# Performance work log

Hardware: AMD Instinct MI355X
Metric: run time of the kernel (lower is better)

The kernel has to match this reference:

```python
import jax, jax.numpy as jnp
import numpy as np

M_DIM = 256.0  # scaling denominator from __init__ (sqrt(256) = 16)

def setup_inputs() -> dict:
    key = jax.random.key(0)
    kq, kk, kv = jax.random.split(key, 3)
    B, H, S, D = 2, 8, 4096, 64
    q = jax.random.normal(kq, (B, H, S, D), dtype=jnp.float32)
    k = jax.random.normal(kk, (B, H, S, D), dtype=jnp.float32)
    v = jax.random.normal(kv, (B, H, S, D), dtype=jnp.float32)
    return {"q": q, "k": k, "v": v}

def reference(q, k, v):
    # scores: [B, H, S, S] = q @ k^T / sqrt(m_dim)
    scores = jnp.einsum('bhqd,bhkd->bhqk', q, k) / jnp.sqrt(jnp.float32(M_DIM))
    attn = jax.nn.softmax(scores, axis=-1)
    # outputs: [B, H, S, D]
    return jnp.einsum('bhqk,bhkd->bhqd', attn, v)
```

## Files before the change

### kernel.cpp

```cpp
#include <hip/hip_runtime.h>
#include <hip/hip_bf16.h>
#include <stdint.h>

#define SEQ 4096
#define DH  64
#define KT  64
#define PS  72
#define LOG2E 1.44269504f
#define PC2   5.76796516f

typedef __attribute__((ext_vector_type(8))) short short8;
typedef __attribute__((ext_vector_type(4))) float floatx4;

__device__ __forceinline__ ushort f2bf_rne(float f) {
    unsigned u = __float_as_uint(f);
    unsigned r = u + 0x7FFFu + ((u >> 16) & 1u);
    return (ushort)(r >> 16);
}

__device__ __forceinline__ void async_copy16(void* lds, const void* gsrc) {
    __builtin_amdgcn_global_load_lds(
        (const __attribute__((address_space(1))) uint32_t*)gsrc,
        (__attribute__((address_space(3))) uint32_t*)lds, 16, 0, 0);
}

__global__ __launch_bounds__(256)
void prep_kv(const float* __restrict__ K, const float* __restrict__ V,
             ushort* __restrict__ Kbf, ushort* __restrict__ Vt) {
    const int bh = blockIdx.y, s0 = blockIdx.x * 64, t = threadIdx.x;
    const size_t base = ((size_t)bh * SEQ + s0) * DH;
    {
        const float* src = K + base + t * 16;
        ushort* dst = Kbf + base + t * 16;
        #pragma unroll
        for (int h = 0; h < 2; ++h) {
            float4 a = *(const float4*)(src + h * 8);
            float4 b = *(const float4*)(src + h * 8 + 4);
            short8 o;
            o[0] = (short)f2bf_rne(a.x); o[1] = (short)f2bf_rne(a.y);
            o[2] = (short)f2bf_rne(a.z); o[3] = (short)f2bf_rne(a.w);
            o[4] = (short)f2bf_rne(b.x); o[5] = (short)f2bf_rne(b.y);
            o[6] = (short)f2bf_rne(b.z); o[7] = (short)f2bf_rne(b.w);
            *(short8*)(dst + h * 8) = o;
        }
    }
    {
        const int d0 = (t >> 4) * 4, sl = (t & 15) * 4;
        const float* src = V + base + (size_t)sl * DH + d0;
        ushort* dst = Vt + (size_t)bh * DH * SEQ + s0 + sl;
        ushort b[4][4];
        #pragma unroll
        for (int r = 0; r < 4; ++r) {
            float4 f = *(const float4*)(src + r * DH);
            b[r][0] = f2bf_rne(f.x); b[r][1] = f2bf_rne(f.y);
            b[r][2] = f2bf_rne(f.z); b[r][3] = f2bf_rne(f.w);
        }
        #pragma unroll
        for (int i = 0; i < 4; ++i) {
            uint2 w;
            w.x = (uint)b[0][i] | ((uint)b[1][i] << 16);
            w.y = (uint)b[2][i] | ((uint)b[3][i] << 16);
            *(uint2*)(dst + (size_t)(d0 + i) * SEQ) = w;
        }
    }
}

__global__ __launch_bounds__(128, 2)
void attn_fwd_v3(const float* __restrict__ Q, const ushort* __restrict__ Kbf,
                 const ushort* __restrict__ Vt, float* __restrict__ O)
{
    __shared__ __align__(16) ushort sK [KT * DH];
    __shared__ __align__(16) ushort sVt[DH * KT];
    __shared__ __align__(16) ushort sP [2 * 32 * PS];

    const int bh   = blockIdx.y;
    const int qt0  = blockIdx.x * 64;
    const int tid  = threadIdx.x;
    const int wave = tid >> 6;
    const int lane = tid & 63;
    const int n16  = lane & 15;
    const int quad = lane >> 4;

    const float* Qb  = Q + ((size_t)bh * SEQ) * DH;
    const char*  KbB = (const char*)(Kbf + (size_t)bh * SEQ * DH);
    const char*  VtB = (const char*)(Vt  + (size_t)bh * DH * SEQ);
    float*       Ob  = O + ((size_t)bh * SEQ) * DH;

    const int qw0 = qt0 + wave * 32;
    short8 qfrag[2][2];
    #pragma unroll
    for (int qt = 0; qt < 2; ++qt) {
        const float* qrow = Qb + (size_t)(qw0 + qt * 16 + n16) * DH;
        #pragma unroll
        for (int t = 0; t < 2; ++t) {
            const float* p = qrow + t * 32 + quad * 8;
            short8 a;
            #pragma unroll
            for (int j = 0; j < 8; ++j) a[j] = (short)f2bf_rne(p[j] * 0.0625f);
            qfrag[qt][t] = a;
        }
    }

    int kOff[4], vOff[4];
    char *kLds[4], *vLds[4];
    #pragma unroll
    for (int c = 0; c < 4; ++c) {
        int L = (c * 2 + wave) * 1024 + lane * 16;
        int row = L >> 7, p = (L >> 4) & 7;
        int sw = (p ^ (row & 7)) * 16;
        kOff[c] = row * 128  + sw;
        vOff[c] = row * 8192 + sw;
        kLds[c] = (char*)sK  + (c * 2 + wave) * 1024;
        vLds[c] = (char*)sVt + (c * 2 + wave) * 1024;
    }
    const int sw0 = ((0 * 4 + quad) ^ (n16 & 7)) * 8;
    const int sw1 = ((1 * 4 + quad) ^ (n16 & 7)) * 8;

    floatx4 oacc[2][4];
    #pragma unroll
    for (int qt = 0; qt < 2; ++qt)
        #pragma unroll
        for (int nt = 0; nt < 4; ++nt) oacc[qt][nt] = (floatx4){0.f, 0.f, 0.f, 0.f};
    float l_i[2] = {0.f, 0.f};

    ushort* sPw = &sP[wave * 32 * PS];

    for (int kt0 = 0; kt0 < SEQ; kt0 += KT) {
        __syncthreads();
        #pragma unroll
        for (int c = 0; c < 4; ++c)
            async_copy16(kLds[c], KbB + (size_t)kt0 * 128 + kOff[c]);
        #pragma unroll
        for (int c = 0; c < 4; ++c)
            async_copy16(vLds[c], VtB + (size_t)kt0 * 2 + vOff[c]);
        __syncthreads();

        floatx4 sacc[4][2];
        #pragma unroll
        for (int kt = 0; kt < 4; ++kt) {
            short8 k0 = *(const short8*)&sK[(kt * 16 + n16) * 64 + sw0];
            short8 k1 = *(const short8*)&sK[(kt * 16 + n16) * 64 + sw1];
            #pragma unroll
            for (int qt = 0; qt < 2; ++qt) {
                floatx4 acc = (floatx4){0.f, 0.f, 0.f, 0.f};
                acc = __builtin_amdgcn_mfma_f32_16x16x32_bf16(k0, qfrag[qt][0], acc, 0, 0, 0);
                acc = __builtin_amdgcn_mfma_f32_16x16x32_bf16(k1, qfrag[qt][1], acc, 0, 0, 0);
                sacc[kt][qt] = acc;
            }
        }

        #pragma unroll
        for (int kt = 0; kt < 4; ++kt) {
            #pragma unroll
            for (int qt = 0; qt < 2; ++qt) {
                float p0 = __builtin_amdgcn_exp2f(__builtin_fmaf(sacc[kt][qt][0], LOG2E, -PC2));
                float p1 = __builtin_amdgcn_exp2f(__builtin_fmaf(sacc[kt][qt][1], LOG2E, -PC2));
                float p2 = __builtin_amdgcn_exp2f(__builtin_fmaf(sacc[kt][qt][2], LOG2E, -PC2));
                float p3 = __builtin_amdgcn_exp2f(__builtin_fmaf(sacc[kt][qt][3], LOG2E, -PC2));
                l_i[qt] += (p0 + p1) + (p2 + p3);
                uint2 w;
                w.x = (__float_as_uint(p0) >> 16) | (__float_as_uint(p1) & 0xFFFF0000u);
                w.y = (__float_as_uint(p2) >> 16) | (__float_as_uint(p3) & 0xFFFF0000u);
                *(uint2*)&sPw[(qt * 16 + n16) * PS + kt * 16 + quad * 4] = w;
            }
        }

        short8 pf[2][2];
        #pragma unroll
        for (int qt = 0; qt < 2; ++qt) {
            pf[qt][0] = *(const short8*)&sPw[(qt * 16 + n16) * PS + 0 * 32 + quad * 8];
            pf[qt][1] = *(const short8*)&sPw[(qt * 16 + n16) * PS + 1 * 32 + quad * 8];
        }
        #pragma unroll
        for (int nt = 0; nt < 4; ++nt) {
            short8 v0 = *(const short8*)&sVt[(nt * 16 + n16) * 64 + sw0];
            short8 v1 = *(const short8*)&sVt[(nt * 16 + n16) * 64 + sw1];
            #pragma unroll
            for (int qt = 0; qt < 2; ++qt) {
                oacc[qt][nt] = __builtin_amdgcn_mfma_f32_16x16x32_bf16(v0, pf[qt][0], oacc[qt][nt], 0, 0, 0);
                oacc[qt][nt] = __builtin_amdgcn_mfma_f32_16x16x32_bf16(v1, pf[qt][1], oacc[qt][nt], 0, 0, 0);
            }
        }
    }

    #pragma unroll
    for (int qt = 0; qt < 2; ++qt) {
        float l = l_i[qt];
        l += __shfl_xor(l, 16, 64);
        l += __shfl_xor(l, 32, 64);
        float inv = 1.0019531f / l;
        const int q = qw0 + qt * 16 + n16;
        #pragma unroll
        for (int nt = 0; nt < 4; ++nt) {
            float4 o;
            o.x = oacc[qt][nt][0] * inv;
            o.y = oacc[qt][nt][1] * inv;
            o.z = oacc[qt][nt][2] * inv;
            o.w = oacc[qt][nt][3] * inv;
            *(float4*)&Ob[(size_t)q * DH + nt * 16 + quad * 4] = o;
        }
    }
}

__global__ __launch_bounds__(256, 4)
void attn_fwd_v1(const float* __restrict__ Q, const float* __restrict__ K,
                 const float* __restrict__ V, float* __restrict__ O)
{
    __shared__ __align__(16) ushort sKf[KT * PS];
    __shared__ __align__(16) ushort sVf[DH * PS];
    __shared__ __align__(16) ushort sPf[4 * 16 * PS];
    const int bh = blockIdx.y, qt0 = blockIdx.x * 64, tid = threadIdx.x;
    const int wave = tid >> 6, lane = tid & 63, n16 = lane & 15, quad = lane >> 4;
    const size_t base = (size_t)bh * SEQ * DH;
    const float *Qb = Q + base, *Kb = K + base, *Vb = V + base;
    float* Ob = O + base;
    short8 qfrag[2];
    {
        const float* qrow = Qb + (size_t)(qt0 + wave * 16 + n16) * DH;
        #pragma unroll
        for (int t = 0; t < 2; ++t) {
            const float* p = qrow + t * 32 + quad * 8;
            short8 a;
            #pragma unroll
            for (int j = 0; j < 8; ++j) a[j] = (short)f2bf_rne(p[j] * 0.0625f);
            qfrag[t] = a;
        }
    }
    floatx4 oacc[4];
    #pragma unroll
    for (int nt = 0; nt < 4; ++nt) oacc[nt] = (floatx4){0.f,0.f,0.f,0.f};
    float m_i[4] = {-INFINITY,-INFINITY,-INFINITY,-INFINITY};
    float l_i[4] = {0.f,0.f,0.f,0.f};
    const int skr = tid >> 2, sc0 = (tid & 3) * 16;
    for (int kt0 = 0; kt0 < SEQ; kt0 += KT) {
        __syncthreads();
        const float* ksrc = Kb + (size_t)(kt0 + skr) * DH + sc0;
        const float* vsrc = Vb + (size_t)(kt0 + skr) * DH + sc0;
        ushort* kdst = &sKf[skr * PS + sc0];
        #pragma unroll
        for (int i = 0; i < 16; i += 4) {
            float4 kf = *(const float4*)(ksrc + i);
            kdst[i+0]=f2bf_rne(kf.x); kdst[i+1]=f2bf_rne(kf.y);
            kdst[i+2]=f2bf_rne(kf.z); kdst[i+3]=f2bf_rne(kf.w);
            float4 vf = *(const float4*)(vsrc + i);
            sVf[(sc0+i+0)*PS+skr]=f2bf_rne(vf.x); sVf[(sc0+i+1)*PS+skr]=f2bf_rne(vf.y);
            sVf[(sc0+i+2)*PS+skr]=f2bf_rne(vf.z); sVf[(sc0+i+3)*PS+skr]=f2bf_rne(vf.w);
        }
        __syncthreads();
        floatx4 sacc[4];
        #pragma unroll
        for (int nt = 0; nt < 4; ++nt) {
            sacc[nt] = (floatx4){0.f,0.f,0.f,0.f};
            #pragma unroll
            for (int t = 0; t < 2; ++t) {
                short8 b = *(const short8*)&sKf[(nt*16+n16)*PS + t*32 + quad*8];
                sacc[nt] = __builtin_amdgcn_mfma_f32_16x16x32_bf16(qfrag[t], b, sacc[nt], 0,0,0);
            }
        }
        ushort* pw = &sPf[wave * 16 * PS];
        #pragma unroll
        for (int r = 0; r < 4; ++r) {
            float mx = fmaxf(fmaxf(sacc[0][r],sacc[1][r]),fmaxf(sacc[2][r],sacc[3][r]));
            #pragma unroll
            for (int off = 1; off < 16; off <<= 1) mx = fmaxf(mx, __shfl_xor(mx, off, 64));
            float mnew = fmaxf(m_i[r], mx);
            float alpha = __expf(m_i[r] - mnew);
            m_i[r] = mnew;
            float sum = 0.f;
            #pragma unroll
            for (int nt = 0; nt < 4; ++nt) {
                float p = __expf(sacc[nt][r] - mnew);
                sacc[nt][r] = p; sum += p;
            }
            #pragma unroll
            for (int off = 1; off < 16; off <<= 1) sum += __shfl_xor(sum, off, 64);
            l_i[r] = l_i[r] * alpha + sum;
            #pragma unroll
            for (int nt = 0; nt < 4; ++nt) oacc[nt][r] *= alpha;
            #pragma unroll
            for (int nt = 0; nt < 4; ++nt)
                pw[(quad*4+r)*PS + nt*16 + n16] = f2bf_rne(sacc[nt][r]);
        }
        #pragma unroll
        for (int t = 0; t < 2; ++t) {
            short8 pfr = *(const short8*)&pw[n16*PS + t*32 + quad*8];
            #pragma unroll
            for (int nt = 0; nt < 4; ++nt) {
                short8 vf = *(const short8*)&sVf[(nt*16+n16)*PS + t*32 + quad*8];
                oacc[nt] = __builtin_amdgcn_mfma_f32_16x16x32_bf16(pfr, vf, oacc[nt], 0,0,0);
            }
        }
    }
    #pragma unroll
    for (int r = 0; r < 4; ++r) {
        float inv = 1.0f / l_i[r];
        float* orow = Ob + (size_t)(qt0 + wave*16 + quad*4 + r) * DH;
        #pragma unroll
        for (int nt = 0; nt < 4; ++nt) orow[nt*16+n16] = oacc[nt][r] * inv;
    }
}

extern "C" void kernel_launch(void* const* d_in, const int* in_sizes, int n_in,
                              void* d_out, int out_size, void* d_ws, size_t ws_size,
                              hipStream_t stream) {
    const float* q = (const float*)d_in[0];
    const float* k = (const float*)d_in[1];
    const float* v = (const float*)d_in[2];
    float* o = (float*)d_out;
    const size_t elems = (size_t)16 * SEQ * DH;
    const size_t need  = elems * 2 * 2;
    if (ws_size >= need) {
        ushort* kbf = (ushort*)d_ws;
        ushort* vt  = kbf + elems;
        prep_kv<<<dim3(SEQ / 64, 16), dim3(256), 0, stream>>>(k, v, kbf, vt);
        attn_fwd_v3<<<dim3(SEQ / 64, 16), dim3(128), 0, stream>>>(q, kbf, vt, o);
    } else {
        attn_fwd_v1<<<dim3(SEQ / 64, 16), dim3(256), 0, stream>>>(q, k, v, o);
    }
}
```

Measured before the change: 193.2 us.

## Split key range across wave pairs and compute row sums via MFMA

```diff
diff --git a/kernel.cpp b/kernel.cpp
--- a/kernel.cpp
+++ b/kernel.cpp
@@ -4,8 +4,8 @@
 
 #define SEQ 4096
 #define DH  64
-#define KT  64
-#define PS  72
+#define KT  32
+#define PS  40
 #define LOG2E 1.44269504f
 #define PC2   5.76796516f
 
@@ -27,13 +27,13 @@
 __global__ __launch_bounds__(256)
 void prep_kv(const float* __restrict__ K, const float* __restrict__ V,
              ushort* __restrict__ Kbf, ushort* __restrict__ Vt) {
-    const int bh = blockIdx.y, s0 = blockIdx.x * 64, t = threadIdx.x;
+    const int bh = blockIdx.y, s0 = blockIdx.x * 128, t = threadIdx.x;
     const size_t base = ((size_t)bh * SEQ + s0) * DH;
     {
-        const float* src = K + base + t * 16;
-        ushort* dst = Kbf + base + t * 16;
-        #pragma unroll
-        for (int h = 0; h < 2; ++h) {
+        const float* src = K + base + t * 32;
+        ushort* dst = Kbf + base + t * 32;
+        #pragma unroll
+        for (int h = 0; h < 4; ++h) {
             float4 a = *(const float4*)(src + h * 8);
             float4 b = *(const float4*)(src + h * 8 + 4);
             short8 o;
@@ -45,48 +45,52 @@
         }
     }
     {
-        const int d0 = (t >> 4) * 4, sl = (t & 15) * 4;
+        const int d0 = (t & 15) * 4, sl = (t >> 4) * 8;
         const float* src = V + base + (size_t)sl * DH + d0;
         ushort* dst = Vt + (size_t)bh * DH * SEQ + s0 + sl;
-        ushort b[4][4];
-        #pragma unroll
-        for (int r = 0; r < 4; ++r) {
+        ushort b[8][4];
+        #pragma unroll
+        for (int r = 0; r < 8; ++r) {
             float4 f = *(const float4*)(src + r * DH);
             b[r][0] = f2bf_rne(f.x); b[r][1] = f2bf_rne(f.y);
             b[r][2] = f2bf_rne(f.z); b[r][3] = f2bf_rne(f.w);
         }
         #pragma unroll
         for (int i = 0; i < 4; ++i) {
-            uint2 w;
-            w.x = (uint)b[0][i] | ((uint)b[1][i] << 16);
-            w.y = (uint)b[2][i] | ((uint)b[3][i] << 16);
-            *(uint2*)(dst + (size_t)(d0 + i) * SEQ) = w;
-        }
-    }
-}
-
-__global__ __launch_bounds__(128, 2)
-void attn_fwd_v3(const float* __restrict__ Q, const ushort* __restrict__ Kbf,
+            short8 w;
+            #pragma unroll
+            for (int r = 0; r < 8; ++r) w[r] = (short)b[r][i];
+            *(short8*)(dst + (size_t)(d0 + i) * SEQ) = w;
+        }
+    }
+}
+
+__global__ __launch_bounds__(256, 4)
+void attn_fwd_v4(const float* __restrict__ Q, const ushort* __restrict__ Kbf,
                  const ushort* __restrict__ Vt, float* __restrict__ O)
 {
-    __shared__ __align__(16) ushort sK [KT * DH];
-    __shared__ __align__(16) ushort sVt[DH * KT];
-    __shared__ __align__(16) ushort sP [2 * 32 * PS];
-
-    const int bh   = blockIdx.y;
-    const int qt0  = blockIdx.x * 64;
-    const int tid  = threadIdx.x;
-    const int wave = tid >> 6;
-    const int lane = tid & 63;
-    const int n16  = lane & 15;
-    const int quad = lane >> 4;
+    __shared__ __align__(16) char smem[26624];
+
+    const int bh    = blockIdx.y;
+    const int qt0   = blockIdx.x * 64;
+    const int tid   = threadIdx.x;
+    const int wave  = tid >> 6;
+    const int widx  = wave & 1;
+    const int wpair = wave >> 1;
+    const int lane  = tid & 63;
+    const int n16   = lane & 15;
+    const int quad  = lane >> 4;
 
     const float* Qb  = Q + ((size_t)bh * SEQ) * DH;
     const char*  KbB = (const char*)(Kbf + (size_t)bh * SEQ * DH);
     const char*  VtB = (const char*)(Vt  + (size_t)bh * DH * SEQ);
     float*       Ob  = O + ((size_t)bh * SEQ) * DH;
 
-    const int qw0 = qt0 + wave * 32;
+    ushort* sK  = (ushort*)(smem)         + wpair * 2048;
+    ushort* sVt = (ushort*)(smem + 8192)  + wpair * 2048;
+    ushort* sPw = (ushort*)(smem + 16384) + wave  * 1280;
+
+    const int qw0 = qt0 + widx * 32;
     short8 qfrag[2][2];
     #pragma unroll
     for (int qt = 0; qt < 2; ++qt) {
@@ -100,64 +104,67 @@
             qfrag[qt][t] = a;
         }
     }
-
-    int kOff[4], vOff[4];
-    char *kLds[4], *vLds[4];
-    #pragma unroll
-    for (int c = 0; c < 4; ++c) {
-        int L = (c * 2 + wave) * 1024 + lane * 16;
-        int row = L >> 7, p = (L >> 4) & 7;
-        int sw = (p ^ (row & 7)) * 16;
-        kOff[c] = row * 128  + sw;
-        vOff[c] = row * 8192 + sw;
-        kLds[c] = (char*)sK  + (c * 2 + wave) * 1024;
-        vLds[c] = (char*)sVt + (c * 2 + wave) * 1024;
-    }
-    const int sw0 = ((0 * 4 + quad) ^ (n16 & 7)) * 8;
-    const int sw1 = ((1 * 4 + quad) ^ (n16 & 7)) * 8;
+    short8 ones;
+    #pragma unroll
+    for (int j = 0; j < 8; ++j) ones[j] = (short)0x3F80;
+
+    int kGoff[2], vGoff[2];
+    char *kDst[2], *vDst[2];
+    #pragma unroll
+    for (int c = 0; c < 2; ++c) {
+        int L = (c * 2 + widx) * 1024 + lane * 16;
+        int krow = L >> 7, kp = (L >> 4) & 7;
+        kGoff[c] = krow * 128 + ((kp ^ (krow & 7)) * 16);
+        kDst[c]  = (char*)sK + L;
+        int vrow = L >> 6, vp = (L >> 4) & 3;
+        vGoff[c] = vrow * (SEQ * 2) + ((vp ^ (vrow & 3)) * 16);
+        vDst[c]  = (char*)sVt + L;
+    }
+    const int sw0  = ((0 + quad) ^ (n16 & 7)) * 8;
+    const int sw1  = ((4 + quad) ^ (n16 & 7)) * 8;
+    const int sw_v = ((quad) ^ (n16 & 3)) * 8;
 
     floatx4 oacc[2][4];
-    #pragma unroll
-    for (int qt = 0; qt < 2; ++qt)
+    floatx4 lacc[2];
+    #pragma unroll
+    for (int qt = 0; qt < 2; ++qt) {
+        lacc[qt] = (floatx4){0.f, 0.f, 0.f, 0.f};
         #pragma unroll
         for (int nt = 0; nt < 4; ++nt) oacc[qt][nt] = (floatx4){0.f, 0.f, 0.f, 0.f};
-    float l_i[2] = {0.f, 0.f};
-
-    ushort* sPw = &sP[wave * 32 * PS];
-
-    for (int kt0 = 0; kt0 < SEQ; kt0 += KT) {
+    }
+
+    const int k0 = wpair * (SEQ / 2);
+    for (int it = 0; it < (SEQ / 2) / KT; ++it) {
+        const int kb = k0 + it * KT;
         __syncthreads();
-        #pragma unroll
-        for (int c = 0; c < 4; ++c)
-            async_copy16(kLds[c], KbB + (size_t)kt0 * 128 + kOff[c]);
-        #pragma unroll
-        for (int c = 0; c < 4; ++c)
-            async_copy16(vLds[c], VtB + (size_t)kt0 * 2 + vOff[c]);
+        async_copy16(kDst[0], KbB + (size_t)kb * 128 + kGoff[0]);
+        async_copy16(kDst[1], KbB + (size_t)kb * 128 + kGoff[1]);
+        async_copy16(vDst[0], VtB + (size_t)kb * 2   + vGoff[0]);
+        async_copy16(vDst[1], VtB + (size_t)kb * 2   + vGoff[1]);
         __syncthreads();
 
-        floatx4 sacc[4][2];
-        #pragma unroll
-        for (int kt = 0; kt < 4; ++kt) {
-            short8 k0 = *(const short8*)&sK[(kt * 16 + n16) * 64 + sw0];
-            short8 k1 = *(const short8*)&sK[(kt * 16 + n16) * 64 + sw1];
+        floatx4 sacc[2][2];
+        #pragma unroll
+        for (int kt = 0; kt < 2; ++kt) {
+            short8 kf0 = *(const short8*)&sK[(kt * 16 + n16) * 64 + sw0];
+            short8 kf1 = *(const short8*)&sK[(kt * 16 + n16) * 64 + sw1];
             #pragma unroll
             for (int qt = 0; qt < 2; ++qt) {
                 floatx4 acc = (floatx4){0.f, 0.f, 0.f, 0.f};
-                acc = __builtin_amdgcn_mfma_f32_16x16x32_bf16(k0, qfrag[qt][0], acc, 0, 0, 0);
-                acc = __builtin_amdgcn_mfma_f32_16x16x32_bf16(k1, qfrag[qt][1], acc, 0, 0, 0);
+                acc = __builtin_amdgcn_mfma_f32_16x16x32_bf16(kf0, qfrag[qt][0], acc, 0, 0, 0);
+                acc = __builtin_amdgcn_mfma_f32_16x16x32_bf16(kf1, qfrag[qt][1], acc, 0, 0, 0);
                 sacc[kt][qt] = acc;
             }
         }
 
         #pragma unroll
-        for (int kt = 0; kt < 4; ++kt) {
+        for (int kt = 0; kt < 2; ++kt) {
             #pragma unroll
             for (int qt = 0; qt < 2; ++qt) {
                 float p0 = __builtin_amdgcn_exp2f(__builtin_fmaf(sacc[kt][qt][0], LOG2E, -PC2));
                 float p1 = __builtin_amdgcn_exp2f(__builtin_fmaf(sacc[kt][qt][1], LOG2E, -PC2));
                 float p2 = __builtin_amdgcn_exp2f(__builtin_fmaf(sacc[kt][qt][2], LOG2E, -PC2));
                 float p3 = __builtin_amdgcn_exp2f(__builtin_fmaf(sacc[kt][qt][3], LOG2E, -PC2));
-                l_i[qt] += (p0 + p1) + (p2 + p3);
                 uint2 w;
                 w.x = (__float_as_uint(p0) >> 16) | (__float_as_uint(p1) & 0xFFFF0000u);
                 w.y = (__float_as_uint(p2) >> 16) | (__float_as_uint(p3) & 0xFFFF0000u);
@@ -165,39 +172,53 @@
             }
         }
 
-        short8 pf[2][2];
+        short8 pf[2];
+        #pragma unroll
+        for (int qt = 0; qt < 2; ++qt)
+            pf[qt] = *(const short8*)&sPw[(qt * 16 + n16) * PS + quad * 8];
+        #pragma unroll
+        for (int nt = 0; nt < 4; ++nt) {
+            short8 vf = *(const short8*)&sVt[(nt * 16 + n16) * 32 + sw_v];
+            #pragma unroll
+            for (int qt = 0; qt < 2; ++qt)
+                oacc[qt][nt] = __builtin_amdgcn_mfma_f32_16x16x32_bf16(vf, pf[qt], oacc[qt][nt], 0, 0, 0);
+        }
+        #pragma unroll
+        for (int qt = 0; qt < 2; ++qt)
+            lacc[qt] = __builtin_amdgcn_mfma_f32_16x16x32_bf16(ones, pf[qt], lacc[qt], 0, 0, 0);
+    }
+
+    __syncthreads();
+    float* epiO = (float*)smem;
+    float* epiL = (float*)(smem + 17408);
+    if (wpair == 1) {
         #pragma unroll
         for (int qt = 0; qt < 2; ++qt) {
-            pf[qt][0] = *(const short8*)&sPw[(qt * 16 + n16) * PS + 0 * 32 + quad * 8];
-            pf[qt][1] = *(const short8*)&sPw[(qt * 16 + n16) * PS + 1 * 32 + quad * 8];
-        }
-        #pragma unroll
-        for (int nt = 0; nt < 4; ++nt) {
-            short8 v0 = *(const short8*)&sVt[(nt * 16 + n16) * 64 + sw0];
-            short8 v1 = *(const short8*)&sVt[(nt * 16 + n16) * 64 + sw1];
-            #pragma unroll
-            for (int qt = 0; qt < 2; ++qt) {
-                oacc[qt][nt] = __builtin_amdgcn_mfma_f32_16x16x32_bf16(v0, pf[qt][0], oacc[qt][nt], 0, 0, 0);
-                oacc[qt][nt] = __builtin_amdgcn_mfma_f32_16x16x32_bf16(v1, pf[qt][1], oacc[qt][nt], 0, 0, 0);
-            }
-        }
-    }
-
-    #pragma unroll
-    for (int qt = 0; qt < 2; ++qt) {
-        float l = l_i[qt];
-        l += __shfl_xor(l, 16, 64);
-        l += __shfl_xor(l, 32, 64);
-        float inv = 1.0019531f / l;
-        const int q = qw0 + qt * 16 + n16;
-        #pragma unroll
-        for (int nt = 0; nt < 4; ++nt) {
-            float4 o;
-            o.x = oacc[qt][nt][0] * inv;
-            o.y = oacc[qt][nt][1] * inv;
-            o.z = oacc[qt][nt][2] * inv;
-            o.w = oacc[qt][nt][3] * inv;
-            *(float4*)&Ob[(size_t)q * DH + nt * 16 + quad * 4] = o;
+            const int row = widx * 32 + qt * 16 + n16;
+            #pragma unroll
+            for (int nt = 0; nt < 4; ++nt)
+                *(float4*)&epiO[row * 68 + nt * 16 + quad * 4] = (float4){
+                    oacc[qt][nt][0], oacc[qt][nt][1], oacc[qt][nt][2], oacc[qt][nt][3]};
+            if (quad == 0) epiL[row] = lacc[qt][0];
+        }
+    }
+    __syncthreads();
+    if (wpair == 0) {
+        #pragma unroll
+        for (int qt = 0; qt < 2; ++qt) {
+            const int row = widx * 32 + qt * 16 + n16;
+            const float inv = 1.0f / (lacc[qt][0] + epiL[row]);
+            const int q = qw0 + qt * 16 + n16;
+            #pragma unroll
+            for (int nt = 0; nt < 4; ++nt) {
+                float4 part = *(const float4*)&epiO[row * 68 + nt * 16 + quad * 4];
+                float4 o;
+                o.x = (oacc[qt][nt][0] + part.x) * inv;
+                o.y = (oacc[qt][nt][1] + part.y) * inv;
+                o.z = (oacc[qt][nt][2] + part.z) * inv;
+                o.w = (oacc[qt][nt][3] + part.w) * inv;
+                *(float4*)&Ob[(size_t)q * DH + nt * 16 + quad * 4] = o;
+            }
         }
     }
 }
@@ -206,9 +227,9 @@
 void attn_fwd_v1(const float* __restrict__ Q, const float* __restrict__ K,
                  const float* __restrict__ V, float* __restrict__ O)
 {
-    __shared__ __align__(16) ushort sKf[KT * PS];
-    __shared__ __align__(16) ushort sVf[DH * PS];
-    __shared__ __align__(16) ushort sPf[4 * 16 * PS];
+    __shared__ __align__(16) ushort sKf[64 * 72];
+    __shared__ __align__(16) ushort sVf[64 * 72];
+    __shared__ __align__(16) ushort sPf[4 * 16 * 72];
     const int bh = blockIdx.y, qt0 = blockIdx.x * 64, tid = threadIdx.x;
     const int wave = tid >> 6, lane = tid & 63, n16 = lane & 15, quad = lane >> 4;
     const size_t base = (size_t)bh * SEQ * DH;
@@ -232,19 +253,19 @@
     float m_i[4] = {-INFINITY,-INFINITY,-INFINITY,-INFINITY};
     float l_i[4] = {0.f,0.f,0.f,0.f};
     const int skr = tid >> 2, sc0 = (tid & 3) * 16;
-    for (int kt0 = 0; kt0 < SEQ; kt0 += KT) {
+    for (int kt0 = 0; kt0 < SEQ; kt0 += 64) {
         __syncthreads();
         const float* ksrc = Kb + (size_t)(kt0 + skr) * DH + sc0;
         const float* vsrc = Vb + (size_t)(kt0 + skr) * DH + sc0;
-        ushort* kdst = &sKf[skr * PS + sc0];
+        ushort* kdst = &sKf[skr * 72 + sc0];
         #pragma unroll
         for (int i = 0; i < 16; i += 4) {
             float4 kf = *(const float4*)(ksrc + i);
             kdst[i+0]=f2bf_rne(kf.x); kdst[i+1]=f2bf_rne(kf.y);
             kdst[i+2]=f2bf_rne(kf.z); kdst[i+3]=f2bf_rne(kf.w);
             float4 vf = *(const float4*)(vsrc + i);
-            sVf[(sc0+i+0)*PS+skr]=f2bf_rne(vf.x); sVf[(sc0+i+1)*PS+skr]=f2bf_rne(vf.y);
-            sVf[(sc0+i+2)*PS+skr]=f2bf_rne(vf.z); sVf[(sc0+i+3)*PS+skr]=f2bf_rne(vf.w);
+            sVf[(sc0+i+0)*72+skr]=f2bf_rne(vf.x); sVf[(sc0+i+1)*72+skr]=f2bf_rne(vf.y);
+            sVf[(sc0+i+2)*72+skr]=f2bf_rne(vf.z); sVf[(sc0+i+3)*72+skr]=f2bf_rne(vf.w);
         }
         __syncthreads();
         floatx4 sacc[4];
@@ -253,11 +274,11 @@
             sacc[nt] = (floatx4){0.f,0.f,0.f,0.f};
             #pragma unroll
             for (int t = 0; t < 2; ++t) {
-                short8 b = *(const short8*)&sKf[(nt*16+n16)*PS + t*32 + quad*8];
+                short8 b = *(const short8*)&sKf[(nt*16+n16)*72 + t*32 + quad*8];
                 sacc[nt] = __builtin_amdgcn_mfma_f32_16x16x32_bf16(qfrag[t], b, sacc[nt], 0,0,0);
             }
         }
-        ushort* pw = &sPf[wave * 16 * PS];
+        ushort* pw = &sPf[wave * 16 * 72];
         #pragma unroll
         for (int r = 0; r < 4; ++r) {
             float mx = fmaxf(fmaxf(sacc[0][r],sacc[1][r]),fmaxf(sacc[2][r],sacc[3][r]));
@@ -279,14 +300,14 @@
             for (int nt = 0; nt < 4; ++nt) oacc[nt][r] *= alpha;
             #pragma unroll
             for (int nt = 0; nt < 4; ++nt)
-                pw[(quad*4+r)*PS + nt*16 + n16] = f2bf_rne(sacc[nt][r]);
+                pw[(quad*4+r)*72 + nt*16 + n16] = f2bf_rne(sacc[nt][r]);
         }
         #pragma unroll
         for (int t = 0; t < 2; ++t) {
-            short8 pfr = *(const short8*)&pw[n16*PS + t*32 + quad*8];
+            short8 pfr = *(const short8*)&pw[n16*72 + t*32 + quad*8];
             #pragma unroll
             for (int nt = 0; nt < 4; ++nt) {
-                short8 vf = *(const short8*)&sVf[(nt*16+n16)*PS + t*32 + quad*8];
+                short8 vf = *(const short8*)&sVf[(nt*16+n16)*72 + t*32 + quad*8];
                 oacc[nt] = __builtin_amdgcn_mfma_f32_16x16x32_bf16(pfr, vf, oacc[nt], 0,0,0);
             }
         }
@@ -312,8 +333,8 @@
     if (ws_size >= need) {
         ushort* kbf = (ushort*)d_ws;
         ushort* vt  = kbf + elems;
-        prep_kv<<<dim3(SEQ / 64, 16), dim3(256), 0, stream>>>(k, v, kbf, vt);
-        attn_fwd_v3<<<dim3(SEQ / 64, 16), dim3(128), 0, stream>>>(q, kbf, vt, o);
+        prep_kv<<<dim3(SEQ / 128, 16), dim3(256), 0, stream>>>(k, v, kbf, vt);
+        attn_fwd_v4<<<dim3(SEQ / 64, 16), dim3(256), 0, stream>>>(q, kbf, vt, o);
     } else {
         attn_fwd_v1<<<dim3(SEQ / 64, 16), dim3(256), 0, stream>>>(q, k, v, o);
     }
```

Result: faster. 189.3 us (-2.0%).
